# Performance work log

Measured on AMD Instinct MI355X. Metric: run time of the kernel, lower is better.

The kernel has to match this reference:

```python
import jax, jax.numpy as jnp
import numpy as np

D_MODEL = 1024
N_HEAD = 16
D_H = D_MODEL // N_HEAD


def setup_inputs() -> dict:
    key = jax.random.key(0)
    ks = jax.random.split(key, 5)
    scale = 1.0 / np.sqrt(D_MODEL)
    x = jax.random.normal(ks[0], (4, 2048, D_MODEL), dtype=jnp.float32)
    # torch nn.Linear weights: shape (out_features, in_features)
    W_qkv = jax.random.uniform(ks[1], (3 * D_MODEL, D_MODEL), dtype=jnp.float32, minval=-scale, maxval=scale)
    b_qkv = jax.random.uniform(ks[2], (3 * D_MODEL,), dtype=jnp.float32, minval=-scale, maxval=scale)
    W_o = jax.random.uniform(ks[3], (D_MODEL, D_MODEL), dtype=jnp.float32, minval=-scale, maxval=scale)
    b_o = jax.random.uniform(ks[4], (D_MODEL,), dtype=jnp.float32, minval=-scale, maxval=scale)
    return {"x": x, "W_qkv": W_qkv, "b_qkv": b_qkv, "W_o": W_o, "b_o": b_o}


def reference(x, W_qkv, b_qkv, W_o, b_o):
    B, S, D = x.shape
    qkv = jnp.einsum('bsd,ed->bse', x, W_qkv) + b_qkv  # [B,S,3D]
    q, k, v = jnp.split(qkv, 3, axis=-1)
    # [B,H,S,d_h]
    q = q.reshape(B, S, N_HEAD, D_H).transpose(0, 2, 1, 3)
    k = k.reshape(B, S, N_HEAD, D_H).transpose(0, 2, 1, 3)
    v = v.reshape(B, S, N_HEAD, D_H).transpose(0, 2, 1, 3)
    sim = jnp.einsum('bhqd,bhkd->bhqk', q, k) / jnp.sqrt(jnp.float32(D_H))
    neg_inf = jnp.finfo(sim.dtype).min
    causal = jnp.tril(jnp.ones((S, S), dtype=bool))
    sim = jnp.where(causal[None, None], sim, neg_inf)
    attn = jax.nn.softmax(sim, axis=-1)
    out = jnp.einsum('bhqk,bhkd->bhqd', attn, v)  # [B,H,S,d_h]
    out = out.transpose(0, 2, 1, 3).reshape(B, S, D)
    return jnp.einsum('bsd,ed->bse', out, W_o) + b_o
```

## Files before the change

### kernel.cpp

```cpp
#include <hip/hip_runtime.h>

#define D_MODEL 1024
#define S_LEN   2048
#define BATCH   4
#define NH      16
#define DH      64
#define M_ROWS  (BATCH * S_LEN)

typedef __attribute__((ext_vector_type(8))) short short8;
typedef __attribute__((ext_vector_type(4))) float floatx4;
typedef unsigned short ushort_t;
typedef __attribute__((ext_vector_type(4))) ushort_t ushortx4;

__device__ __forceinline__ ushort_t f2bf(float f) {
    union { float f; unsigned u; } v; v.f = f;
    unsigned r = v.u + 0x7FFFu + ((v.u >> 16) & 1u);
    return (ushort_t)(r >> 16);
}

__device__ __forceinline__ int pack2(float lo, float hi) {
    return (int)__builtin_amdgcn_perm(__float_as_uint(hi), __float_as_uint(lo), 0x07060302u);
}

__device__ __forceinline__ void async_copy16(const ushort_t* g, ushort_t* l) {
    __builtin_amdgcn_global_load_lds(
        (const __attribute__((address_space(1))) void*)g,
        (__attribute__((address_space(3))) void*)l,
        16, 0, 0);
}

#define N0 (M_ROWS * D_MODEL)
#define N1 (3 * D_MODEL * D_MODEL)
#define N2 (D_MODEL * D_MODEL)
#define NQUADS ((N0 + N1 + N2) / 4)

__global__ __launch_bounds__(256)
void cvt_f32_bf16(const float* __restrict__ s0, const float* __restrict__ s1,
                  const float* __restrict__ s2, ushort_t* __restrict__ d0,
                  ushort_t* __restrict__ d1, ushort_t* __restrict__ d2)
{
    const int q = blockIdx.x * 256 + threadIdx.x;
    if (q >= NQUADS) return;
    const float* s; ushort_t* d; int e;
    if (q < N0 / 4)            { s = s0; d = d0; e = q * 4; }
    else if (q < (N0 + N1) / 4){ s = s1; d = d1; e = q * 4 - N0; }
    else                       { s = s2; d = d2; e = q * 4 - N0 - N1; }
    const float4 v = *(const float4*)&s[e];
    ushortx4 o;
    o[0] = f2bf(v.x); o[1] = f2bf(v.y); o[2] = f2bf(v.z); o[3] = f2bf(v.w);
    *(ushortx4*)&d[e] = o;
}

template<bool F32OUT, bool VSPLIT>
__global__ __launch_bounds__(512, 2)
void gemm_pipe(const ushort_t* __restrict__ A, const ushort_t* __restrict__ B,
               const float* __restrict__ bias, void* __restrict__ Cv,
               ushort_t* __restrict__ vt, int M, int N, int K)
{
    constexpr int BM = 256;
    constexpr int BN = 128;
    constexpr int BK = 64;
    constexpr float C2 = 0.18033688011112042f;
    __shared__ ushort_t As[3][BM][BK];
    __shared__ ushort_t Bs[3][BN][BK];

    const int tid  = threadIdx.x;
    const int lane = tid & 63;
    const int wave = tid >> 6;
    const int quad = lane >> 4;
    const int l16  = lane & 15;
    const int l8r  = lane >> 3;
    const int c8   = lane & 7;
    const int swz  = l16 & 7;

    const int gdx = gridDim.x;
    const int bid = blockIdx.y * gdx + blockIdx.x;
    const int nwg = gdx * gridDim.y;
    const int sw  = (bid & 7) * (nwg >> 3) + (bid >> 3);
    const int bm  = (sw / gdx) * BM;
    const int bn  = (sw % gdx) * BN;

    const int wm = (wave & 3) * 64;
    const int wn = (wave >> 2) * 64;

    const int NT = K >> 6;

    auto STAGE = [&](int s, int kt) {
        const int k0 = kt * BK;
        const int cc = (c8 ^ l8r) * 8;
        #pragma unroll
        for (int i = 0; i < 4; i++) {
            const int rb = (i * 8 + wave) * 8;
            async_copy16(&A[(size_t)(bm + rb + l8r) * K + k0 + cc], &As[s][rb][0]);
        }
        #pragma unroll
        for (int i = 0; i < 2; i++) {
            const int rb = (i * 8 + wave) * 8;
            async_copy16(&B[(size_t)(bn + rb + l8r) * K + k0 + cc], &Bs[s][rb][0]);
        }
    };

    STAGE(0, 0);
    STAGE(1, 1);

    floatx4 acc[4][4] = {};

    for (int t = 0; t < NT; t++) {
        if (t + 1 < NT) {
            asm volatile("s_waitcnt vmcnt(6)" ::: "memory");
        } else {
            asm volatile("s_waitcnt vmcnt(0)" ::: "memory");
        }
        __builtin_amdgcn_s_barrier();
        if (t + 2 < NT) STAGE((t + 2) % 3, t + 2);

        const int s = t % 3;
        #pragma unroll
        for (int h = 0; h < 2; h++) {
            short8 af[4], bfr[4];
            #pragma unroll
            for (int i = 0; i < 4; i++)
                af[i]  = *(const short8*)&As[s][wm + i * 16 + l16][((h * 4 + quad) ^ swz) * 8];
            #pragma unroll
            for (int i = 0; i < 4; i++)
                bfr[i] = *(const short8*)&Bs[s][wn + i * 16 + l16][((h * 4 + quad) ^ swz) * 8];

            #pragma unroll
            for (int mi = 0; mi < 4; mi++)
                #pragma unroll
                for (int ni = 0; ni < 4; ni++)
                    acc[mi][ni] = __builtin_amdgcn_mfma_f32_16x16x32_bf16(af[mi], bfr[ni], acc[mi][ni], 0, 0, 0);
        }
    }

    #pragma unroll
    for (int ni = 0; ni < 4; ni++) {
        const int col = bn + wn + ni * 16 + l16;
        const float bv = bias[col];
        #pragma unroll
        for (int mi = 0; mi < 4; mi++)
            #pragma unroll
            for (int r = 0; r < 4; r++) {
                const int row = bm + wm + mi * 16 + quad * 4 + r;
                const float val = acc[mi][ni][r] + bv;
                if (VSPLIT) {
                    if (col < 2 * D_MODEL) {
                        const float vv = (col < D_MODEL) ? val * C2 : val;
                        ((ushort_t*)Cv)[(size_t)row * 2048 + col] = f2bf(vv);
                    } else {
                        const int vcol = col - 2 * D_MODEL;
                        const int h = vcol >> 6, dh = vcol & 63;
                        const int b = row >> 11, s2 = row & 2047;
                        const int sp = (s2 & ~63) | ((s2 & 15) << 2) | ((s2 >> 4) & 3);
                        vt[(((size_t)(b * NH + h)) * DH + dh) * S_LEN + sp] = f2bf(val);
                    }
                } else if (F32OUT) {
                    ((float*)Cv)[(size_t)row * N + col] = val;
                } else {
                    ((ushort_t*)Cv)[(size_t)row * N + col] = f2bf(val);
                }
            }
    }
}

#define BKV 64

struct TileState {
    short8  qf[2];
    floatx4 o[4];
    float   l[4];
};

__device__ __forceinline__ void attn_tile(
    const ushort_t (*__restrict__ Ks)[DH], const ushort_t (*__restrict__ Vs)[BKV],
    ushort_t* __restrict__ Psw, TileState& st, bool diag,
    int wave, int quad, int l16, int swz, short8 ones)
{
    floatx4 sc[4];
    __builtin_amdgcn_s_setprio(1);
    #pragma unroll
    for (int ns = 0; ns < 4; ns++) {
        const short8 kf0 = *(const short8*)&Ks[ns * 16 + l16][(quad ^ swz) * 8];
        const short8 kf1 = *(const short8*)&Ks[ns * 16 + l16][((4 + quad) ^ swz) * 8];
        floatx4 z = {};
        z = __builtin_amdgcn_mfma_f32_16x16x32_bf16(st.qf[0], kf0, z, 0, 0, 0);
        z = __builtin_amdgcn_mfma_f32_16x16x32_bf16(st.qf[1], kf1, z, 0, 0, 0);
        sc[ns] = z;
    }
    __builtin_amdgcn_s_setprio(0);

    #pragma unroll
    for (int r = 0; r < 4; r++) {
        const int qloc = wave * 16 + quad * 4 + r;
        float p[4];
        #pragma unroll
        for (int ns = 0; ns < 4; ns++) {
            float v = sc[ns][r];
            if (diag) {
                const int kj = ns * 16 + l16;
                v = (kj <= qloc) ? v : -1e30f;
            }
            p[ns] = __builtin_amdgcn_exp2f(v);
        }
        int2 w;
        w.x = pack2(p[0], p[1]);
        w.y = pack2(p[2], p[3]);
        const int row = quad * 4 + r;
        *(int2*)((char*)Psw + row * 128 + (((l16 >> 1) ^ (row & 7)) << 4) + ((l16 & 1) << 3)) = w;
    }

    short8 pf[2];
    #pragma unroll
    for (int c = 0; c < 2; c++)
        pf[c] = *(const short8*)((const char*)Psw + l16 * 128 + ((((c << 2) | quad) ^ (l16 & 7)) << 4));

    __builtin_amdgcn_s_setprio(1);
    floatx4 racc = {};
    racc = __builtin_amdgcn_mfma_f32_16x16x32_bf16(pf[0], ones, racc, 0, 0, 0);
    racc = __builtin_amdgcn_mfma_f32_16x16x32_bf16(pf[1], ones, racc, 0, 0, 0);

    #pragma unroll
    for (int r = 0; r < 4; r++)
        st.l[r] += racc[r];

    #pragma unroll
    for (int d = 0; d < 4; d++) {
        #pragma unroll
        for (int c = 0; c < 2; c++) {
            const short8 vf = *(const short8*)&Vs[d * 16 + l16][((c * 4 + quad) ^ swz) * 8];
            st.o[d] = __builtin_amdgcn_mfma_f32_16x16x32_bf16(pf[c], vf, st.o[d], 0, 0, 0);
        }
    }
    __builtin_amdgcn_s_setprio(0);
}

__device__ __forceinline__ void stage_tile(
    const ushort_t* __restrict__ kg, const ushort_t* __restrict__ vg, int kb,
    ushort_t (*__restrict__ Ksb)[DH], ushort_t (*__restrict__ Vsb)[BKV],
    int wave, int l8r, int c8)
{
    #pragma unroll
    for (int i = wave; i < 8; i += 4) {
        const int row = i * 8 + l8r;
        const int cc  = (c8 ^ l8r) * 8;
        async_copy16(&kg[(size_t)(kb + row) * 2048 + cc], &Ksb[i * 8][0]);
        async_copy16(&vg[(size_t)row * S_LEN + kb + cc], &Vsb[i * 8][0]);
    }
}

__global__ __launch_bounds__(256, 4)
void attn_causal(const ushort_t* __restrict__ qk, const ushort_t* __restrict__ vt,
                 ushort_t* __restrict__ out)
{
    __shared__ ushort_t Ks[2][BKV][DH];
    __shared__ ushort_t Vs[2][DH][BKV];
    __shared__ ushort_t Ps[4][16][64];

    const int tid  = threadIdx.x;
    const int lane = tid & 63;
    const int wave = tid >> 6;
    const int quad = lane >> 4;
    const int l16  = lane & 15;
    const int l8r  = lane >> 3;
    const int c8   = lane & 7;
    const int swz  = l16 & 7;

    const int id  = blockIdx.y * 16 + blockIdx.x;
    const int sid = (id & 7) * 128 + (id >> 3);
    const int qa  = sid & 15;
    const int qb  = 31 - qa;
    const int bh  = sid >> 4;
    const int b   = bh >> 4;
    const int h   = bh & 15;

    const size_t qkbase = (size_t)b * S_LEN * 2048;
    const ushort_t* kg = qk + qkbase + D_MODEL + h * DH;
    const ushort_t* vg = vt + (size_t)(b * NH + h) * DH * S_LEN;

    TileState sa, sb;
    #pragma unroll
    for (int r = 0; r < 4; r++) { sa.l[r] = 0.f; sb.l[r] = 0.f; }
    #pragma unroll
    for (int d = 0; d < 4; d++) { sa.o[d] = (floatx4){}; sb.o[d] = (floatx4){}; }

    {
        const ushort_t* qpa = qk + qkbase + (size_t)(qa * 64 + wave * 16 + l16) * 2048 + h * DH;
        sa.qf[0] = *(const short8*)(qpa + quad * 8);
        sa.qf[1] = *(const short8*)(qpa + 32 + quad * 8);
        const ushort_t* qpb = qk + qkbase + (size_t)(qb * 64 + wave * 16 + l16) * 2048 + h * DH;
        sb.qf[0] = *(const short8*)(qpb + quad * 8);
        sb.qf[1] = *(const short8*)(qpb + 32 + quad * 8);
    }

    short8 ones;
    #pragma unroll
    for (int j = 0; j < 8; j++) ones[j] = (short)0x3F80;

    stage_tile(kg, vg, 0, Ks[0], Vs[0], wave, l8r, c8);

    int cur = 0;
    for (int t = 0; t <= qb; t++) {
        __syncthreads();
        if (t < qb)
            stage_tile(kg, vg, (t + 1) * BKV, Ks[cur ^ 1], Vs[cur ^ 1], wave, l8r, c8);

        if (t <= qa) attn_tile(Ks[cur], Vs[cur], &Ps[wave][0][0], sa, t == qa, wave, quad, l16, swz, ones);
        attn_tile(Ks[cur], Vs[cur], &Ps[wave][0][0], sb, t == qb, wave, quad, l16, swz, ones);
        cur ^= 1;
    }

    #pragma unroll
    for (int r = 0; r < 4; r++) {
        const float inva = 1.0f / sa.l[r];
        const float invb = 1.0f / sb.l[r];
        const int ra = qa * 64 + wave * 16 + quad * 4 + r;
        const int rb = qb * 64 + wave * 16 + quad * 4 + r;
        #pragma unroll
        for (int d = 0; d < 4; d++) {
            out[(size_t)(b * S_LEN + ra) * D_MODEL + h * DH + d * 16 + l16] = f2bf(sa.o[d][r] * inva);
            out[(size_t)(b * S_LEN + rb) * D_MODEL + h * DH + d * 16 + l16] = f2bf(sb.o[d][r] * invb);
        }
    }
}

extern "C" void kernel_launch(void* const* d_in, const int* in_sizes, int n_in,
                              void* d_out, int out_size, void* d_ws, size_t ws_size,
                              hipStream_t stream)
{
    const float* x    = (const float*)d_in[0];
    const float* Wqkv = (const float*)d_in[1];
    const float* bqkv = (const float*)d_in[2];
    const float* Wo   = (const float*)d_in[3];
    const float* bo   = (const float*)d_in[4];
    float* out = (float*)d_out;

    ushort_t* xb    = (ushort_t*)d_ws;
    ushort_t* wqkvb = xb + N0;
    ushort_t* wob   = wqkvb + N1;
    ushort_t* qkbuf = wob + N2;
    ushort_t* vtbuf = qkbuf + (size_t)M_ROWS * 2048;
    ushort_t* att   = vtbuf + (size_t)BATCH * NH * DH * S_LEN;

    cvt_f32_bf16<<<dim3((NQUADS + 255) / 256), dim3(256), 0, stream>>>(x, Wqkv, Wo, xb, wqkvb, wob);
    gemm_pipe<false, true>
        <<<dim3((3 * D_MODEL) / 128, M_ROWS / 256), dim3(512), 0, stream>>>(
        xb, wqkvb, bqkv, qkbuf, vtbuf, M_ROWS, 3 * D_MODEL, D_MODEL);
    attn_causal<<<dim3(16, BATCH * NH), dim3(256), 0, stream>>>(qkbuf, vtbuf, att);
    gemm_pipe<true, false>
        <<<dim3(D_MODEL / 128, M_ROWS / 256), dim3(512), 0, stream>>>(
        att, wob, bo, out, nullptr, M_ROWS, D_MODEL, D_MODEL);
}
```

Before: 269.2 us.

## Restructure GEMM pipeline to 6-slot BK=32 ring with 128x256 tiles

```diff
diff --git a/kernel.cpp b/kernel.cpp
--- a/kernel.cpp
+++ b/kernel.cpp
@@ -57,21 +57,18 @@
                const float* __restrict__ bias, void* __restrict__ Cv,
                ushort_t* __restrict__ vt, int M, int N, int K)
 {
-    constexpr int BM = 256;
-    constexpr int BN = 128;
-    constexpr int BK = 64;
+    constexpr int BM = 128;
+    constexpr int BN = 256;
+    constexpr int BK = 32;
+    constexpr int SLOT = 12288;
     constexpr float C2 = 0.18033688011112042f;
-    __shared__ ushort_t As[3][BM][BK];
-    __shared__ ushort_t Bs[3][BN][BK];
+    __shared__ ushort_t lds[6 * SLOT];
 
     const int tid  = threadIdx.x;
     const int lane = tid & 63;
     const int wave = tid >> 6;
     const int quad = lane >> 4;
     const int l16  = lane & 15;
-    const int l8r  = lane >> 3;
-    const int c8   = lane & 7;
-    const int swz  = l16 & 7;
 
     const int gdx = gridDim.x;
     const int bid = blockIdx.y * gdx + blockIdx.x;
@@ -80,57 +77,64 @@
     const int bm  = (sw / gdx) * BM;
     const int bn  = (sw % gdx) * BN;
 
-    const int wm = (wave & 3) * 64;
-    const int wn = (wave >> 2) * 64;
-
-    const int NT = K >> 6;
-
-    auto STAGE = [&](int s, int kt) {
-        const int k0 = kt * BK;
-        const int cc = (c8 ^ l8r) * 8;
-        #pragma unroll
-        for (int i = 0; i < 4; i++) {
-            const int rb = (i * 8 + wave) * 8;
-            async_copy16(&A[(size_t)(bm + rb + l8r) * K + k0 + cc], &As[s][rb][0]);
-        }
-        #pragma unroll
-        for (int i = 0; i < 2; i++) {
-            const int rb = (i * 8 + wave) * 8;
-            async_copy16(&B[(size_t)(bn + rb + l8r) * K + k0 + cc], &Bs[s][rb][0]);
-        }
+    const int wm = (wave & 1) * 64;
+    const int wn = (wave >> 1) * 64;
+
+    const int NT = K / BK;
+
+    const int srow = lane >> 2;
+    const int gch  = ((lane & 3) ^ (srow & 3)) << 3;
+    const ushort_t* ag  = &A[(size_t)(bm +       wave * 16 + srow) * K + gch];
+    const ushort_t* bg0 = &B[(size_t)(bn +       wave * 16 + srow) * K + gch];
+    const ushort_t* bg1 = &B[(size_t)(bn + 128 + wave * 16 + srow) * K + gch];
+    ushort_t* ald  = &lds[wave * 512];
+    ushort_t* bld0 = &lds[4096 + wave * 512];
+    ushort_t* bld1 = &lds[8192 + wave * 512];
+
+    auto STAGE = [&](int kt) {
+        const int so = (kt % 6) * SLOT;
+        const int ko = kt * BK;
+        async_copy16(ag  + ko, ald  + so);
+        async_copy16(bg0 + ko, bld0 + so);
+        async_copy16(bg1 + ko, bld1 + so);
     };
 
-    STAGE(0, 0);
-    STAGE(1, 1);
+    STAGE(0); STAGE(1); STAGE(2); STAGE(3);
+    asm volatile("s_waitcnt vmcnt(9)" ::: "memory");
+    __builtin_amdgcn_s_barrier();
+    asm volatile("" ::: "memory");
 
     floatx4 acc[4][4] = {};
+    const int rsw = (l16 & 3);
 
     for (int t = 0; t < NT; t++) {
-        if (t + 1 < NT) {
-            asm volatile("s_waitcnt vmcnt(6)" ::: "memory");
-        } else {
-            asm volatile("s_waitcnt vmcnt(0)" ::: "memory");
-        }
+        const int so = (t % 6) * SLOT;
+        short8 af[4], bf[4];
+        #pragma unroll
+        for (int i = 0; i < 4; i++)
+            af[i] = *(const short8*)&lds[so + (wm + i * 16 + l16) * 32 + ((quad ^ rsw) << 3)];
+        #pragma unroll
+        for (int i = 0; i < 4; i++)
+            bf[i] = *(const short8*)&lds[so + 4096 + (wn + i * 16 + l16) * 32 + ((quad ^ rsw) << 3)];
+
+        if (t + 4 < NT) STAGE(t + 4);
+
+        const int rem = NT - 2 - t;
+        if (rem >= 3)      asm volatile("s_waitcnt vmcnt(9)" ::: "memory");
+        else if (rem == 2) asm volatile("s_waitcnt vmcnt(6)" ::: "memory");
+        else if (rem == 1) asm volatile("s_waitcnt vmcnt(3)" ::: "memory");
+        else               asm volatile("s_waitcnt vmcnt(0)" ::: "memory");
         __builtin_amdgcn_s_barrier();
-        if (t + 2 < NT) STAGE((t + 2) % 3, t + 2);
-
-        const int s = t % 3;
-        #pragma unroll
-        for (int h = 0; h < 2; h++) {
-            short8 af[4], bfr[4];
+        asm volatile("" ::: "memory");
+
+        __builtin_amdgcn_s_setprio(1);
+        #pragma unroll
+        for (int mi = 0; mi < 4; mi++)
             #pragma unroll
-            for (int i = 0; i < 4; i++)
-                af[i]  = *(const short8*)&As[s][wm + i * 16 + l16][((h * 4 + quad) ^ swz) * 8];
-            #pragma unroll
-            for (int i = 0; i < 4; i++)
-                bfr[i] = *(const short8*)&Bs[s][wn + i * 16 + l16][((h * 4 + quad) ^ swz) * 8];
-
-            #pragma unroll
-            for (int mi = 0; mi < 4; mi++)
-                #pragma unroll
-                for (int ni = 0; ni < 4; ni++)
-                    acc[mi][ni] = __builtin_amdgcn_mfma_f32_16x16x32_bf16(af[mi], bfr[ni], acc[mi][ni], 0, 0, 0);
-        }
+            for (int ni = 0; ni < 4; ni++)
+                acc[mi][ni] = __builtin_amdgcn_mfma_f32_16x16x32_bf16(af[mi], bf[ni], acc[mi][ni], 0, 0, 0);
+        __builtin_amdgcn_s_setprio(0);
+        asm volatile("" ::: "memory");
     }
 
     #pragma unroll
@@ -343,10 +347,10 @@
 
     cvt_f32_bf16<<<dim3((NQUADS + 255) / 256), dim3(256), 0, stream>>>(x, Wqkv, Wo, xb, wqkvb, wob);
     gemm_pipe<false, true>
-        <<<dim3((3 * D_MODEL) / 128, M_ROWS / 256), dim3(512), 0, stream>>>(
+        <<<dim3((3 * D_MODEL) / 256, M_ROWS / 128), dim3(512), 0, stream>>>(
         xb, wqkvb, bqkv, qkbuf, vtbuf, M_ROWS, 3 * D_MODEL, D_MODEL);
     attn_causal<<<dim3(16, BATCH * NH), dim3(256), 0, stream>>>(qkbuf, vtbuf, att);
     gemm_pipe<true, false>
-        <<<dim3(D_MODEL / 128, M_ROWS / 256), dim3(512), 0, stream>>>(
+        <<<dim3(D_MODEL / 256, M_ROWS / 128), dim3(512), 0, stream>>>(
         att, wob, bo, out, nullptr, M_ROWS, D_MODEL, D_MODEL);
 }
```

Result: no change. 271.8 us (+1.0%).
